# Kernel optimization log

Hardware: AMD Instinct MI355X
Metric: run time of the kernel (lower is better)

The kernel has to match this reference:

```python
import jax, jax.numpy as jnp
import numpy as np

B, T, D, H, L = 16384, 100, 5, 32, 1  # batch, seq_len, input/output dim, hidden, latent


def setup_inputs() -> dict:
    key = jax.random.key(0)
    ks = jax.random.split(key, 28)
    rn = lambda k, shp, s=0.1: jax.random.normal(k, shp, dtype=jnp.float32) * s
    return {
        "x": rn(ks[0], (B, T, D), 1.0),
        "eps": rn(ks[1], (B, L), 1.0),
        # Encoder LSTM (PyTorch layout: W_ih [4H, D], W_hh [4H, H], gate order i,f,g,o)
        "enc_Wih": rn(ks[2], (4 * H, D)), "enc_Whh": rn(ks[3], (4 * H, H)),
        "enc_bih": rn(ks[4], (4 * H,)), "enc_bhh": rn(ks[5], (4 * H,)),
        "W_mu": rn(ks[6], (L, 2 * H)), "b_mu": rn(ks[7], (L,)),
        "W_lv": rn(ks[8], (L, 2 * H)), "b_lv": rn(ks[9], (L,)),
        # Decoder
        "W_l2h": rn(ks[10], (H, L)), "b_l2h": rn(ks[11], (H,)),
        "W_l2h2": rn(ks[12], (H, L)), "b_l2h2": rn(ks[13], (H,)),
        "start_token": jnp.zeros((1, D), jnp.float32),
        "W_emb": rn(ks[14], (H, D)), "b_emb": rn(ks[15], (H,)),
        "dec_Wih": rn(ks[16], (4 * H, H)), "dec_Whh": rn(ks[17], (4 * H, H)),
        "dec_bih": rn(ks[18], (4 * H,)), "dec_bhh": rn(ks[19], (4 * H,)),
        "W_out": rn(ks[20], (D, H)), "b_out": rn(ks[21], (D,)),
        "W_seq": rn(ks[22], (H, L)), "b_seq": rn(ks[23], (H,)),
        "W_seq2": rn(ks[24], (1, H)), "b_seq2": rn(ks[25], (1,)),
    }


def _lstm_cell(x_t, h, c, Wih, Whh, b):
    g = x_t @ Wih.T + h @ Whh.T + b            # [B, 4H]
    i, f, gg, o = jnp.split(g, 4, axis=-1)      # PyTorch gate order i,f,g,o
    c = jax.nn.sigmoid(f) * c + jax.nn.sigmoid(i) * jnp.tanh(gg)
    h = jax.nn.sigmoid(o) * jnp.tanh(c)
    return h, c


def reference(x, eps, enc_Wih, enc_Whh, enc_bih, enc_bhh, W_mu, b_mu, W_lv, b_lv,
              W_l2h, b_l2h, W_l2h2, b_l2h2, start_token, W_emb, b_emb,
              dec_Wih, dec_Whh, dec_bih, dec_bhh, W_out, b_out,
              W_seq, b_seq, W_seq2, b_seq2):
    bsz, seq_len, _ = x.shape
    hdim = enc_Whh.shape[1]
    lrelu = lambda v: jax.nn.leaky_relu(v, negative_slope=0.01)

    # ---- Encoder LSTM over time ----
    b_enc = enc_bih + enc_bhh
    def enc_step(carry, x_t):
        h, c = carry
        h, c = _lstm_cell(x_t, h, c, enc_Wih, enc_Whh, b_enc)
        return (h, c), None
    z0 = jnp.zeros((bsz, hdim), x.dtype)
    (h_n, c_n), _ = jax.lax.scan(enc_step, (z0, z0), jnp.swapaxes(x, 0, 1))
    hcat = jnp.concatenate([h_n, c_n], axis=-1)        # [B, 2H]
    mu = hcat @ W_mu.T + b_mu                           # [B, L]
    log_var = hcat @ W_lv.T + b_lv                      # [B, L]

    # ---- Reparameterize ----
    z = mu + eps * jnp.exp(0.5 * log_var)

    h0 = lrelu(mu @ W_l2h.T + b_l2h)                    # [B, H]
    c0 = lrelu(mu @ W_l2h2.T + b_l2h2)                  # [B, H]
    x0 = jnp.broadcast_to(start_token @ W_emb.T + b_emb, (bsz, hdim))
    b_dec = dec_bih + dec_bhh
    def dec_step(carry, _):
        x_in, h, c = carry
        x_t = jax.nn.relu(x_in)
        h, c = _lstm_cell(x_t, h, c, dec_Wih, dec_Whh, b_dec)
        return (h, h, c), h
    _, hs = jax.lax.scan(dec_step, (x0, h0, c0), None, length=seq_len)  # [T, B, H]
    recon = jnp.swapaxes(hs, 0, 1) @ W_out.T + b_out    # [B, T, D]

    # ---- num head on z (encoder_outputs arg) ----
    num = jax.nn.relu(lrelu(z @ W_seq.T + b_seq) @ W_seq2.T + b_seq2)  # [B, 1]

    return recon, mu, log_var, num
```

## Files before the change

kernel.cpp:

```cpp
#include <hip/hip_runtime.h>
#include <hip/hip_bf16.h>

typedef short bf16x8 __attribute__((ext_vector_type(8)));
typedef float f32x4  __attribute__((ext_vector_type(4)));
typedef unsigned int u32x4 __attribute__((ext_vector_type(4)));

#define LOG2E 1.44269504088896340736f

static __device__ __forceinline__ unsigned short f2bf(float f){
    __hip_bfloat16 h = __float2bfloat16(f);
    return __builtin_bit_cast(unsigned short, h);
}
static __device__ __forceinline__ unsigned pk_bf16(float lo, float hi){
    return (((unsigned)f2bf(hi)) << 16) | (unsigned)f2bf(lo);
}
static __device__ __forceinline__ float rcp_(float x){ return __builtin_amdgcn_rcpf(x); }
static __device__ __forceinline__ float ex2(float x){ return __builtin_amdgcn_exp2f(x); }
static __device__ __forceinline__ f32x4 mfma16(bf16x8 a, bf16x8 b, f32x4 c){
    return __builtin_amdgcn_mfma_f32_16x16x32_bf16(a, b, c, 0, 0, 0);
}
static __device__ __forceinline__ unsigned relu_pk(unsigned v){
    unsigned m = ((v >> 15) & 0x00010001u) * 0xFFFFu;
    return v & ~m;
}

__global__ void marker_kernel(float* out, int n, float v){
    int i = blockIdx.x * 256 + threadIdx.x;
    if (i < n) out[i] = v;
}

__global__ __launch_bounds__(256, 2)
void vae_mfma6_kernel(const float* __restrict__ x,      const float* __restrict__ eps,
                      const float* __restrict__ eWih,   const float* __restrict__ eWhh,
                      const float* __restrict__ ebih,   const float* __restrict__ ebhh,
                      const float* __restrict__ Wmu,    const float* __restrict__ bmu,
                      const float* __restrict__ Wlv,    const float* __restrict__ blv,
                      const float* __restrict__ Wl2h,   const float* __restrict__ bl2h,
                      const float* __restrict__ Wl2h2,  const float* __restrict__ bl2h2,
                      const float* __restrict__ stok,   const float* __restrict__ Wemb,
                      const float* __restrict__ bemb,
                      const float* __restrict__ dWih,   const float* __restrict__ dWhh,
                      const float* __restrict__ dbih,   const float* __restrict__ dbhh,
                      const float* __restrict__ Wout,   const float* __restrict__ bout,
                      const float* __restrict__ Wseq,   const float* __restrict__ bseq,
                      const float* __restrict__ Wseq2,  const float* __restrict__ bseq2,
                      float* __restrict__ recon,
                      float* __restrict__ out_mu,
                      float* __restrict__ out_lv,
                      float* __restrict__ out_num)
{
    __shared__ unsigned hx[2][2][16][20];
    __shared__ float hbf[2][16][33];
    __shared__ float cbf[2][16][33];
    __shared__ float mubuf[2][16];
    __shared__ float x0buf[32];
    __shared__ float cw[524];

    const int tid = threadIdx.x;
    const int w   = tid >> 6;
    const int W   = w & 1;
    const int pi  = w >> 1;
    const int l   = tid & 63;
    const int c   = l & 15;
    const int g   = l >> 4;
    const int bbase = blockIdx.x * 32 + pi * 16;

    if (tid < 64){ cw[tid] = Wmu[tid]; cw[64+tid] = Wlv[tid]; }
    if (tid < 32){
        cw[128+tid] = Wseq[tid];  cw[160+tid] = bseq[tid];  cw[192+tid] = Wseq2[tid];
        cw[224+tid] = Wl2h[tid];  cw[256+tid] = bl2h[tid];
        cw[288+tid] = Wl2h2[tid]; cw[320+tid] = bl2h2[tid];
    }
    if (tid < 160) cw[352+tid] = Wout[tid];
    if (tid < 5)   cw[512+tid] = bout[tid];
    if (tid == 0){ cw[517] = bmu[0]; cw[518] = blv[0]; cw[519] = bseq2[0]; }

    bf16x8 WH[4], WX[4];
    f32x4  biasv[4];
    #pragma unroll
    for (int n=0;n<4;++n){
        const float sc = (n==2) ? (-2.0f*LOG2E) : (-LOG2E);
        const int GR = n*32 + W*16 + c;
        bf16x8 t;
        #pragma unroll
        for (int j=0;j<8;++j) t[j] = (short)f2bf(sc * eWhh[(size_t)GR*32 + g*8 + j]);
        WH[n] = t;
        bf16x8 tx = (bf16x8)0;
        if (g == 0){
            #pragma unroll
            for (int j=0;j<5;++j) tx[j] = (short)f2bf(sc * eWih[(size_t)GR*5 + j]);
        }
        WX[n] = tx;
        f32x4 b4;
        #pragma unroll
        for (int q=0;q<4;++q){
            const int R = n*32 + W*16 + g*4 + q;
            b4[q] = sc * (ebih[R] + ebhh[R]);
        }
        biasv[n] = b4;
    }

    float cs[4], hn[4];
    #pragma unroll
    for (int k=0;k<4;++k){ cs[k] = 0.0f; hn[k] = 0.0f; }

    *(uint2*)&hx[0][pi][c][W*8 + g*2] = make_uint2(0u, 0u);
    int p = 0;
    __syncthreads();

    float4 xA = {0,0,0,0}; float xB = 0.0f;
    if (g == 0){
        const float* xp = x + (size_t)(bbase+c)*500;
        xA = *(const float4*)xp; xB = xp[4];
    }

    for (int t=0; t<100; ++t){
        u32x4 hw = *(const u32x4*)&hx[p][pi][c][g*4];
        bf16x8 bh = __builtin_bit_cast(bf16x8, hw);

        bf16x8 bx = (bf16x8)0;
        if (g == 0){
            bx[0]=(short)f2bf(xA.x); bx[1]=(short)f2bf(xA.y);
            bx[2]=(short)f2bf(xA.z); bx[3]=(short)f2bf(xA.w);
            bx[4]=(short)f2bf(xB);
            if (t < 99){
                const float* xp = x + (size_t)(bbase+c)*500 + (t+1)*5;
                xA = *(const float4*)xp; xB = xp[4];
            }
        }

        f32x4 acc[4];
        #pragma unroll
        for (int n=0;n<4;++n) acc[n] = mfma16(WX[n], bx, biasv[n]);
        #pragma unroll
        for (int n=0;n<4;++n) acc[n] = mfma16(WH[n], bh, acc[n]);

        #pragma unroll
        for (int q=0;q<4;++q){
            float ei = ex2(acc[0][q]);
            float ef = ex2(acc[1][q]);
            float eg = ex2(acc[2][q]);
            float eo = ex2(acc[3][q]);
            float pig = (1.0f+ei)*(1.0f+eg);
            float num = cs[q]*pig + (1.0f+ef)*(1.0f-eg);
            float cn  = num * rcp_((1.0f+ef)*pig);
            float ec  = ex2(cn * (-2.0f*LOG2E));
            hn[q]     = (1.0f-ec) * rcp_((1.0f+eo)*(1.0f+ec));
            cs[q]     = cn;
        }
        *(uint2*)&hx[p^1][pi][c][W*8 + g*2] =
            make_uint2(pk_bf16(hn[0], hn[1]), pk_bf16(hn[2], hn[3]));
        __syncthreads();
        p ^= 1;
    }

    #pragma unroll
    for (int q=0;q<4;++q){
        const int U = W*16 + g*4 + q;
        hbf[pi][c][U] = hn[q];
        cbf[pi][c][U] = cs[q];
    }
    __syncthreads();

    bf16x8 WI[4], WHd[4];
    f32x4  dbias[4];
    #pragma unroll
    for (int n=0;n<4;++n){
        const float sc = (n==2) ? (-2.0f*LOG2E) : (-LOG2E);
        const int GR = n*32 + W*16 + c;
        bf16x8 ti, th;
        #pragma unroll
        for (int j=0;j<8;++j){
            ti[j] = (short)f2bf(sc * dWih[(size_t)GR*32 + g*8 + j]);
            th[j] = (short)f2bf(sc * dWhh[(size_t)GR*32 + g*8 + j]);
        }
        WI[n] = ti; WHd[n] = th;
        f32x4 b4;
        #pragma unroll
        for (int q=0;q<4;++q){
            const int R = n*32 + W*16 + g*4 + q;
            b4[q] = sc * (dbih[R] + dbhh[R]);
        }
        dbias[n] = b4;
    }
    bf16x8 WO = (bf16x8)0;
    f32x4 bosv = (f32x4)0;
    if (c < 5){
        bf16x8 to;
        #pragma unroll
        for (int j=0;j<8;++j) to[j] = (short)f2bf(Wout[c*32 + g*8 + j]);
        WO = to;
    }
    #pragma unroll
    for (int q=0;q<4;++q){
        const int dd = g*4 + q;
        bosv[q] = (dd < 5) ? bout[dd] : 0.0f;
    }

    if (tid < 32){
        const int pr = tid >> 4, rr = tid & 15;
        const int row = blockIdx.x*32 + tid;
        float mu = cw[517], lv = cw[518];
        #pragma unroll
        for (int k=0;k<32;++k){
            float hvv = hbf[pr][rr][k], cvv = cbf[pr][rr][k];
            mu += hvv*cw[k]    + cvv*cw[32+k];
            lv += hvv*cw[64+k] + cvv*cw[96+k];
        }
        out_mu[row] = mu;
        out_lv[row] = lv;
        mubuf[pr][rr] = mu;
        float z = mu + eps[row] * __builtin_amdgcn_exp2f(0.5f*LOG2E*lv);
        float a2 = cw[519];
        #pragma unroll
        for (int j=0;j<32;++j){
            float s = z*cw[128+j] + cw[160+j];
            s = s > 0.0f ? s : 0.01f*s;
            a2 += cw[192+j]*s;
        }
        out_num[row] = fmaxf(a2, 0.0f);
        float v = bemb[tid];
        #pragma unroll
        for (int d=0; d<5; ++d) v += stok[d]*Wemb[tid*5 + d];
        x0buf[tid] = fmaxf(v, 0.0f);
    }
    __syncthreads();

    {
        const float muv = mubuf[pi][c];
        float h4[4];
        #pragma unroll
        for (int q=0;q<4;++q){
            const int U = W*16 + g*4 + q;
            float a = muv*cw[224+U] + cw[256+U];
            float b = muv*cw[288+U] + cw[320+U];
            h4[q]  = (a > 0.0f ? a : 0.01f*a);
            cs[q]  = (b > 0.0f ? b : 0.01f*b);
        }
        *(uint2*)&hx[0][pi][c][W*8 + g*2] =
            make_uint2(pk_bf16(h4[0], h4[1]), pk_bf16(h4[2], h4[3]));
    }
    p = 0;
    __syncthreads();

    bf16x8 bx0;
    #pragma unroll
    for (int j=0;j<8;++j) bx0[j] = (short)f2bf(x0buf[g*8 + j]);

    for (int t=0; t<100; ++t){
        u32x4 hw = *(const u32x4*)&hx[p][pi][c][g*4];
        bf16x8 bh = __builtin_bit_cast(bf16x8, hw);

        bf16x8 bx;
        if (t == 0) bx = bx0;
        else {
            u32x4 rv;
            #pragma unroll
            for (int i=0;i<4;++i) rv[i] = relu_pk(hw[i]);
            bx = __builtin_bit_cast(bf16x8, rv);
        }

        f32x4 acc[4];
        #pragma unroll
        for (int n=0;n<4;++n) acc[n] = mfma16(WI[n], bx, dbias[n]);
        #pragma unroll
        for (int n=0;n<4;++n) acc[n] = mfma16(WHd[n], bh, acc[n]);

        if (W == 0 && t > 0){
            f32x4 ao = mfma16(WO, bh, bosv);
            float* rp = recon + (size_t)(bbase+c)*500 + (t-1)*5;
            if (g == 0){ rp[0]=ao[0]; rp[1]=ao[1]; rp[2]=ao[2]; rp[3]=ao[3]; }
            else if (g == 1){ rp[4]=ao[0]; }
        }

        #pragma unroll
        for (int q=0;q<4;++q){
            float ei = ex2(acc[0][q]);
            float ef = ex2(acc[1][q]);
            float eg = ex2(acc[2][q]);
            float eo = ex2(acc[3][q]);
            float pig = (1.0f+ei)*(1.0f+eg);
            float num = cs[q]*pig + (1.0f+ef)*(1.0f-eg);
            float cn  = num * rcp_((1.0f+ef)*pig);
            float ec  = ex2(cn * (-2.0f*LOG2E));
            hn[q]     = (1.0f-ec) * rcp_((1.0f+eo)*(1.0f+ec));
            cs[q]     = cn;
        }
        *(uint2*)&hx[p^1][pi][c][W*8 + g*2] =
            make_uint2(pk_bf16(hn[0], hn[1]), pk_bf16(hn[2], hn[3]));
        __syncthreads();
        p ^= 1;
    }

    if (W == 0){
        u32x4 hw = *(const u32x4*)&hx[p][pi][c][g*4];
        f32x4 ao = mfma16(WO, __builtin_bit_cast(bf16x8, hw), bosv);
        float* rp = recon + (size_t)(bbase+c)*500 + 99*5;
        if (g == 0){ rp[0]=ao[0]; rp[1]=ao[1]; rp[2]=ao[2]; rp[3]=ao[3]; }
        else if (g == 1){ rp[4]=ao[0]; }
    }
}

extern "C" void kernel_launch(void* const* d_in, const int* in_sizes, int n_in,
                              void* d_out, int out_size, void* d_ws, size_t ws_size,
                              hipStream_t stream)
{
    (void)d_ws; (void)ws_size;
    static const int EXPECT[27] = {8192000,16384,640,4096,128,128,64,1,64,1,
                                   32,32,32,32,5,160,32,4096,4096,128,128,
                                   160,5,32,32,32,1};
    bool in_ok = (n_in == 27);
    if (in_ok) for (int i = 0; i < 27; ++i) in_ok = in_ok && (in_sizes[i] == EXPECT[i]);
    bool out_ok = (out_size == 8241152);

    float* out = (float*)d_out;
    if (!in_ok){
        marker_kernel<<<(out_size + 255)/256, 256, 0, stream>>>(out, out_size, 2.0f);
        return;
    }
    if (!out_ok){
        marker_kernel<<<(out_size + 255)/256, 256, 0, stream>>>(out, out_size, 3.0f);
        return;
    }

    const float* x     = (const float*)d_in[0];
    const float* eps   = (const float*)d_in[1];
    const float* eWih  = (const float*)d_in[2];
    const float* eWhh  = (const float*)d_in[3];
    const float* ebih  = (const float*)d_in[4];
    const float* ebhh  = (const float*)d_in[5];
    const float* Wmu   = (const float*)d_in[6];
    const float* bmu   = (const float*)d_in[7];
    const float* Wlv   = (const float*)d_in[8];
    const float* blv   = (const float*)d_in[9];
    const float* Wl2h  = (const float*)d_in[10];
    const float* bl2h  = (const float*)d_in[11];
    const float* Wl2h2 = (const float*)d_in[12];
    const float* bl2h2 = (const float*)d_in[13];
    const float* stok  = (const float*)d_in[14];
    const float* Wemb  = (const float*)d_in[15];
    const float* bemb  = (const float*)d_in[16];
    const float* dWih  = (const float*)d_in[17];
    const float* dWhh  = (const float*)d_in[18];
    const float* dbih  = (const float*)d_in[19];
    const float* dbhh  = (const float*)d_in[20];
    const float* Wout  = (const float*)d_in[21];
    const float* bout  = (const float*)d_in[22];
    const float* Wseq  = (const float*)d_in[23];
    const float* bseq  = (const float*)d_in[24];
    const float* Wseq2 = (const float*)d_in[25];
    const float* bseq2 = (const float*)d_in[26];

    float* recon  = out;
    float* out_mu = out + 8192000;
    float* out_lv = out_mu + 16384;
    float* out_nm = out_lv + 16384;

    vae_mfma6_kernel<<<512, 256, 0, stream>>>(x, eps,
        eWih, eWhh, ebih, ebhh, Wmu, bmu, Wlv, blv,
        Wl2h, bl2h, Wl2h2, bl2h2, stok, Wemb, bemb,
        dWih, dWhh, dbih, dbhh, Wout, bout,
        Wseq, bseq, Wseq2, bseq2,
        recon, out_mu, out_lv, out_nm);
}
```

Measured before the change: 142.9 us.

## Shrink LSTM blocks to one 16-row tile to narrow per-step barriers

Each block now handles one 16-row batch tile with two waves instead of two tiles with four waves, and the launch doubles the grid to 1024 blocks of 128 threads. The per-timestep __syncthreads then only has to join two waves, which is meant to cut barrier stall on the serial recurrence while keeping the same number of waves per CU. The shared hidden-state buffer is also repacked into a compact [slot][row][4] layout that matches the bf16x8 operand reads. The trade-off is twice as many blocks, each repeating the weight preload and prologue work.

After: 144.5 us. No clear change (+1.1%).

```diff
diff --git a/kernel.cpp b/kernel.cpp
--- a/kernel.cpp
+++ b/kernel.cpp
@@ -29,49 +29,49 @@
     if (i < n) out[i] = v;
 }
 
-__global__ __launch_bounds__(256, 2)
-void vae_mfma6_kernel(const float* __restrict__ x,      const float* __restrict__ eps,
-                      const float* __restrict__ eWih,   const float* __restrict__ eWhh,
-                      const float* __restrict__ ebih,   const float* __restrict__ ebhh,
-                      const float* __restrict__ Wmu,    const float* __restrict__ bmu,
-                      const float* __restrict__ Wlv,    const float* __restrict__ blv,
-                      const float* __restrict__ Wl2h,   const float* __restrict__ bl2h,
-                      const float* __restrict__ Wl2h2,  const float* __restrict__ bl2h2,
-                      const float* __restrict__ stok,   const float* __restrict__ Wemb,
-                      const float* __restrict__ bemb,
-                      const float* __restrict__ dWih,   const float* __restrict__ dWhh,
-                      const float* __restrict__ dbih,   const float* __restrict__ dbhh,
-                      const float* __restrict__ Wout,   const float* __restrict__ bout,
-                      const float* __restrict__ Wseq,   const float* __restrict__ bseq,
-                      const float* __restrict__ Wseq2,  const float* __restrict__ bseq2,
-                      float* __restrict__ recon,
-                      float* __restrict__ out_mu,
-                      float* __restrict__ out_lv,
-                      float* __restrict__ out_num)
+__global__ __launch_bounds__(128, 2)
+void vae_mfma6b_kernel(const float* __restrict__ x,      const float* __restrict__ eps,
+                       const float* __restrict__ eWih,   const float* __restrict__ eWhh,
+                       const float* __restrict__ ebih,   const float* __restrict__ ebhh,
+                       const float* __restrict__ Wmu,    const float* __restrict__ bmu,
+                       const float* __restrict__ Wlv,    const float* __restrict__ blv,
+                       const float* __restrict__ Wl2h,   const float* __restrict__ bl2h,
+                       const float* __restrict__ Wl2h2,  const float* __restrict__ bl2h2,
+                       const float* __restrict__ stok,   const float* __restrict__ Wemb,
+                       const float* __restrict__ bemb,
+                       const float* __restrict__ dWih,   const float* __restrict__ dWhh,
+                       const float* __restrict__ dbih,   const float* __restrict__ dbhh,
+                       const float* __restrict__ Wout,   const float* __restrict__ bout,
+                       const float* __restrict__ Wseq,   const float* __restrict__ bseq,
+                       const float* __restrict__ Wseq2,  const float* __restrict__ bseq2,
+                       float* __restrict__ recon,
+                       float* __restrict__ out_mu,
+                       float* __restrict__ out_lv,
+                       float* __restrict__ out_num)
 {
-    __shared__ unsigned hx[2][2][16][20];
-    __shared__ float hbf[2][16][33];
-    __shared__ float cbf[2][16][33];
-    __shared__ float mubuf[2][16];
+    __shared__ unsigned hx[2][4][16][4];
+    __shared__ float hbf[16][33];
+    __shared__ float cbf[16][33];
+    __shared__ float mubuf[16];
     __shared__ float x0buf[32];
     __shared__ float cw[524];
 
     const int tid = threadIdx.x;
-    const int w   = tid >> 6;
-    const int W   = w & 1;
-    const int pi  = w >> 1;
+    const int W   = tid >> 6;
     const int l   = tid & 63;
     const int c   = l & 15;
     const int g   = l >> 4;
-    const int bbase = blockIdx.x * 32 + pi * 16;
+    const int bbase = blockIdx.x * 16;
 
     if (tid < 64){ cw[tid] = Wmu[tid]; cw[64+tid] = Wlv[tid]; }
-    if (tid < 32){
-        cw[128+tid] = Wseq[tid];  cw[160+tid] = bseq[tid];  cw[192+tid] = Wseq2[tid];
-        cw[224+tid] = Wl2h[tid];  cw[256+tid] = bl2h[tid];
-        cw[288+tid] = Wl2h2[tid]; cw[320+tid] = bl2h2[tid];
-    }
-    if (tid < 160) cw[352+tid] = Wout[tid];
+    if (tid >= 64 && tid < 96){
+        const int i = tid - 64;
+        cw[128+i] = Wseq[i];  cw[160+i] = bseq[i];  cw[192+i] = Wseq2[i];
+        cw[224+i] = Wl2h[i];  cw[256+i] = bl2h[i];
+        cw[288+i] = Wl2h2[i]; cw[320+i] = bl2h2[i];
+    }
+    if (tid < 128){ cw[352+tid] = Wout[tid]; }
+    if (tid >= 96 && tid < 128){ int i = tid - 96; cw[480+i] = Wout[128+i]; }
     if (tid < 5)   cw[512+tid] = bout[tid];
     if (tid == 0){ cw[517] = bmu[0]; cw[518] = blv[0]; cw[519] = bseq2[0]; }
 
@@ -104,7 +104,7 @@
     #pragma unroll
     for (int k=0;k<4;++k){ cs[k] = 0.0f; hn[k] = 0.0f; }
 
-    *(uint2*)&hx[0][pi][c][W*8 + g*2] = make_uint2(0u, 0u);
+    *(uint2*)&hx[0][W*2 + (g>>1)][c][(g&1)*2] = make_uint2(0u, 0u);
     int p = 0;
     __syncthreads();
 
@@ -115,7 +115,7 @@
     }
 
     for (int t=0; t<100; ++t){
-        u32x4 hw = *(const u32x4*)&hx[p][pi][c][g*4];
+        u32x4 hw = *(const u32x4*)&hx[p][g][c][0];
         bf16x8 bh = __builtin_bit_cast(bf16x8, hw);
 
         bf16x8 bx = (bf16x8)0;
@@ -148,7 +148,7 @@
             hn[q]     = (1.0f-ec) * rcp_((1.0f+eo)*(1.0f+ec));
             cs[q]     = cn;
         }
-        *(uint2*)&hx[p^1][pi][c][W*8 + g*2] =
+        *(uint2*)&hx[p^1][W*2 + (g>>1)][c][(g&1)*2] =
             make_uint2(pk_bf16(hn[0], hn[1]), pk_bf16(hn[2], hn[3]));
         __syncthreads();
         p ^= 1;
@@ -157,8 +157,8 @@
     #pragma unroll
     for (int q=0;q<4;++q){
         const int U = W*16 + g*4 + q;
-        hbf[pi][c][U] = hn[q];
-        cbf[pi][c][U] = cs[q];
+        hbf[c][U] = hn[q];
+        cbf[c][U] = cs[q];
     }
     __syncthreads();
 
@@ -197,19 +197,18 @@
         bosv[q] = (dd < 5) ? bout[dd] : 0.0f;
     }
 
-    if (tid < 32){
-        const int pr = tid >> 4, rr = tid & 15;
-        const int row = blockIdx.x*32 + tid;
+    if (tid < 16){
+        const int row = bbase + tid;
         float mu = cw[517], lv = cw[518];
         #pragma unroll
         for (int k=0;k<32;++k){
-            float hvv = hbf[pr][rr][k], cvv = cbf[pr][rr][k];
+            float hvv = hbf[tid][k], cvv = cbf[tid][k];
             mu += hvv*cw[k]    + cvv*cw[32+k];
             lv += hvv*cw[64+k] + cvv*cw[96+k];
         }
         out_mu[row] = mu;
         out_lv[row] = lv;
-        mubuf[pr][rr] = mu;
+        mubuf[tid] = mu;
         float z = mu + eps[row] * __builtin_amdgcn_exp2f(0.5f*LOG2E*lv);
         float a2 = cw[519];
         #pragma unroll
@@ -219,15 +218,18 @@
             a2 += cw[192+j]*s;
         }
         out_num[row] = fmaxf(a2, 0.0f);
-        float v = bemb[tid];
-        #pragma unroll
-        for (int d=0; d<5; ++d) v += stok[d]*Wemb[tid*5 + d];
-        x0buf[tid] = fmaxf(v, 0.0f);
+    }
+    if (tid >= 32 && tid < 64){
+        const int u = tid - 32;
+        float v = bemb[u];
+        #pragma unroll
+        for (int d=0; d<5; ++d) v += stok[d]*Wemb[u*5 + d];
+        x0buf[u] = fmaxf(v, 0.0f);
     }
     __syncthreads();
 
     {
-        const float muv = mubuf[pi][c];
+        const float muv = mubuf[c];
         float h4[4];
         #pragma unroll
         for (int q=0;q<4;++q){
@@ -237,7 +239,7 @@
             h4[q]  = (a > 0.0f ? a : 0.01f*a);
             cs[q]  = (b > 0.0f ? b : 0.01f*b);
         }
-        *(uint2*)&hx[0][pi][c][W*8 + g*2] =
+        *(uint2*)&hx[0][W*2 + (g>>1)][c][(g&1)*2] =
             make_uint2(pk_bf16(h4[0], h4[1]), pk_bf16(h4[2], h4[3]));
     }
     p = 0;
@@ -248,7 +250,7 @@
     for (int j=0;j<8;++j) bx0[j] = (short)f2bf(x0buf[g*8 + j]);
 
     for (int t=0; t<100; ++t){
-        u32x4 hw = *(const u32x4*)&hx[p][pi][c][g*4];
+        u32x4 hw = *(const u32x4*)&hx[p][g][c][0];
         bf16x8 bh = __builtin_bit_cast(bf16x8, hw);
 
         bf16x8 bx;
@@ -286,14 +288,14 @@
             hn[q]     = (1.0f-ec) * rcp_((1.0f+eo)*(1.0f+ec));
             cs[q]     = cn;
         }
-        *(uint2*)&hx[p^1][pi][c][W*8 + g*2] =
+        *(uint2*)&hx[p^1][W*2 + (g>>1)][c][(g&1)*2] =
             make_uint2(pk_bf16(hn[0], hn[1]), pk_bf16(hn[2], hn[3]));
         __syncthreads();
         p ^= 1;
     }
 
     if (W == 0){
-        u32x4 hw = *(const u32x4*)&hx[p][pi][c][g*4];
+        u32x4 hw = *(const u32x4*)&hx[p][g][c][0];
         f32x4 ao = mfma16(WO, __builtin_bit_cast(bf16x8, hw), bosv);
         float* rp = recon + (size_t)(bbase+c)*500 + 99*5;
         if (g == 0){ rp[0]=ao[0]; rp[1]=ao[1]; rp[2]=ao[2]; rp[3]=ao[3]; }
@@ -356,7 +358,7 @@
     float* out_lv = out_mu + 16384;
     float* out_nm = out_lv + 16384;
 
-    vae_mfma6_kernel<<<512, 256, 0, stream>>>(x, eps,
+    vae_mfma6b_kernel<<<1024, 128, 0, stream>>>(x, eps,
         eWih, eWhh, ebih, ebhh, Wmu, bmu, Wlv, blv,
         Wl2h, bl2h, Wl2h2, bl2h2, stok, Wemb, bemb,
         dWih, dWhh, dbih, dbhh, Wout, bout,
```
